# Kernel tuning notes

Measured on AMD Instinct MI355X. Metric: run time of the kernel, lower is better.

The kernel has to match this reference:

```python
import jax, jax.numpy as jnp
import numpy as np

N_PE = 100000   # num 'pe' nodes
N_R = 100000    # num 'router' nodes
E = 600000      # edges per relation
D_IN = 64       # input feature dim per node type
H = 128         # hidden_channels
G = 64          # graphs in batch


def setup_inputs() -> dict:
    key = jax.random.key(0)
    ks = jax.random.split(key, 20)
    inp = {}
    inp["x_pe"] = jax.random.normal(ks[0], (N_PE, D_IN), jnp.float32)
    inp["x_r"] = jax.random.normal(ks[1], (N_R, D_IN), jnp.float32)
    # edge_index per relation: row0 = src node ids, row1 = dst node ids
    inp["ei_per"] = jax.random.randint(ks[2], (2, E), 0, N_PE, jnp.int32)   # pe -> router
    inp["ei_rpe"] = jax.random.randint(ks[3], (2, E), 0, N_R, jnp.int32)    # router -> pe
    inp["ei_rr"] = jax.random.randint(ks[4], (2, E), 0, N_R, jnp.int32)     # router -> router
    inp["batch_pe"] = jnp.sort(jax.random.randint(ks[5], (N_PE,), 0, G, jnp.int32))
    inp["batch_r"] = jnp.sort(jax.random.randint(ks[6], (N_R,), 0, G, jnp.int32))
    # GraphConv params, relation axis ordered [pe->router, router->pe, router->router]
    s1 = 1.0 / np.sqrt(D_IN)
    s2 = 1.0 / np.sqrt(H)
    inp["Wrel1"] = jax.random.normal(ks[7], (3, D_IN, H), jnp.float32) * s1
    inp["brel1"] = jnp.zeros((3, H), jnp.float32)
    inp["Wroot1"] = jax.random.normal(ks[8], (3, D_IN, H), jnp.float32) * s1
    inp["Wrel23"] = jax.random.normal(ks[9], (2, 3, H, H), jnp.float32) * s2
    inp["brel23"] = jnp.zeros((2, 3, H), jnp.float32)
    inp["Wroot23"] = jax.random.normal(ks[10], (2, 3, H, H), jnp.float32) * s2
    # per-node-type MLP heads, type axis ordered [pe, router]
    inp["mlp_W1"] = jax.random.normal(ks[11], (2, H, 5), jnp.float32) * s2
    inp["mlp_b1"] = jnp.zeros((2, 5), jnp.float32)
    inp["mlp_W2"] = jax.random.normal(ks[12], (2, 5, 1), jnp.float32) * (1.0 / np.sqrt(5.0))
    inp["mlp_b2"] = jnp.zeros((2, 1), jnp.float32)
    inp["out_W"] = jax.random.normal(ks[13], (2, 1), jnp.float32) * (1.0 / np.sqrt(2.0))
    inp["out_b"] = jnp.zeros((1,), jnp.float32)
    return inp


def _hetero_graphconv(x_pe, x_r, ei_per, ei_rpe, ei_rr, Wrel, brel, Wroot):
    # GraphConv: lin_rel(scatter_add(x_src)) + lin_root(x_dst); to_hetero sums per dst type.
    agg_r_from_pe = jax.ops.segment_sum(x_pe[ei_per[0]], ei_per[1], num_segments=N_R)
    agg_pe_from_r = jax.ops.segment_sum(x_r[ei_rpe[0]], ei_rpe[1], num_segments=N_PE)
    agg_r_from_r = jax.ops.segment_sum(x_r[ei_rr[0]], ei_rr[1], num_segments=N_R)
    o_pe = agg_pe_from_r @ Wrel[1] + brel[1] + x_pe @ Wroot[1]
    o_r = (agg_r_from_pe @ Wrel[0] + brel[0] + x_r @ Wroot[0]) \
        + (agg_r_from_r @ Wrel[2] + brel[2] + x_r @ Wroot[2])
    return o_pe, o_r


def reference(x_pe, x_r, ei_per, ei_rpe, ei_rr, batch_pe, batch_r,
              Wrel1, brel1, Wroot1, Wrel23, brel23, Wroot23,
              mlp_W1, mlp_b1, mlp_W2, mlp_b2, out_W, out_b):
    h_pe, h_r = _hetero_graphconv(x_pe, x_r, ei_per, ei_rpe, ei_rr, Wrel1, brel1, Wroot1)
    h_pe, h_r = jax.nn.relu(h_pe), jax.nn.relu(h_r)
    h_pe, h_r = _hetero_graphconv(h_pe, h_r, ei_per, ei_rpe, ei_rr, Wrel23[0], brel23[0], Wroot23[0])
    h_pe, h_r = jax.nn.relu(h_pe), jax.nn.relu(h_r)
    h_pe, h_r = _hetero_graphconv(h_pe, h_r, ei_per, ei_rpe, ei_rr, Wrel23[1], brel23[1], Wroot23[1])
    gm_pe = jax.ops.segment_max(h_pe, batch_pe, num_segments=G)  # [G, H]
    gm_r = jax.ops.segment_max(h_r, batch_r, num_segments=G)
    def mlp(x, W1, b1, W2, b2):
        return jax.nn.relu(x @ W1 + b1) @ W2 + b2
    o_pe = mlp(gm_pe, mlp_W1[0], mlp_b1[0], mlp_W2[0], mlp_b2[0])  # [G, 1]
    o_r = mlp(gm_r, mlp_W1[1], mlp_b1[1], mlp_W2[1], mlp_b2[1])
    cat = jnp.concatenate([o_pe, o_r], axis=1)  # [G, 2]
    return cat @ out_W + out_b  # [G, 1]
```

## Files before the change

kernel.cpp:

```cpp
#include <hip/hip_runtime.h>
#include <cstddef>
#include <cstdint>

#define DIN 64
#define HID 128
#define NBKMAX 256
#define EPB 8192

typedef _Float16 half4v __attribute__((ext_vector_type(4)));
typedef _Float16 half8v __attribute__((ext_vector_type(8)));
typedef float f32x16 __attribute__((ext_vector_type(16)));

__device__ __forceinline__ unsigned encf(float f) {
    unsigned b = __float_as_uint(f);
    return (b & 0x80000000u) ? ~b : (b | 0x80000000u);
}
__device__ __forceinline__ float decf(unsigned u) {
    unsigned b = (u & 0x80000000u) ? (u & 0x7FFFFFFFu) : ~u;
    return __uint_as_float(b);
}

__global__ void matadd3_k(const float* a0, const float* b0f, float* o0, int n0,
                          const float* a1, const float* b1f, float* o1, int n1,
                          const float* a2, const float* b2f, float* o2, int n2) {
    int r = blockIdx.y;
    const float* a = r == 0 ? a0 : (r == 1 ? a1 : a2);
    const float* b = r == 0 ? b0f : (r == 1 ? b1f : b2f);
    float* o = r == 0 ? o0 : (r == 1 ? o1 : o2);
    int n = r == 0 ? n0 : (r == 1 ? n1 : n2);
    int i = blockIdx.x * 256 + threadIdx.x;
    if (i < n) o[i] = a[i] + b[i];
}

__global__ void conv_x2_k(const float* s0, _Float16* d0, int n40,
                          const float* s1, _Float16* d1, int n41) {
    int r = blockIdx.y;
    const float* s = r == 0 ? s0 : s1;
    _Float16* d = r == 0 ? d0 : d1;
    int n4 = r == 0 ? n40 : n41;
    int i = blockIdx.x * 256 + threadIdx.x;
    if (i >= n4) return;
    float4 v = *reinterpret_cast<const float4*>(&s[i * 4]);
    half4v h;
    h.x = (_Float16)v.x; h.y = (_Float16)v.y; h.z = (_Float16)v.z; h.w = (_Float16)v.w;
    *reinterpret_cast<half4v*>(&d[i * 4]) = h;
}

struct CW { const float* src; _Float16* dst; int K; int total; };
__global__ void conv_w7_k(CW c0, CW c1, CW c2, CW c3, CW c4, CW c5, CW c6) {
    CW J;
    switch (blockIdx.y) {
        case 0: J = c0; break; case 1: J = c1; break; case 2: J = c2; break;
        case 3: J = c3; break; case 4: J = c4; break; case 5: J = c5; break;
        default: J = c6; break;
    }
    int i = blockIdx.x * 256 + threadIdx.x;
    if (i >= J.total) return;
    int m = i / (J.K * HID);
    int rem = i % (J.K * HID);
    int k = rem / HID;
    int col = rem % HID;
    J.dst[(size_t)m * HID * J.K + (size_t)col * J.K + k] = (_Float16)J.src[i];
}

__global__ __launch_bounds__(256) void bhist_k(const int* e0, const int* e1, const int* e2, int E,
                                               int* c0, int* c1, int* c2) {
    int r = blockIdx.y;
    const int* ei = r == 0 ? e0 : (r == 1 ? e1 : e2);
    int* cnt = r == 0 ? c0 : (r == 1 ? c1 : c2);
    __shared__ int sc[NBKMAX];
    int t = threadIdx.x;
    sc[t] = 0;
    __syncthreads();
    int base = blockIdx.x * EPB;
    int n = min(EPB, E - base);
    for (int i = t; i < n; i += 256)
        atomicAdd(&sc[(unsigned)ei[E + base + i] >> 9], 1);
    __syncthreads();
    if (sc[t]) atomicAdd(&cnt[t], sc[t]);
}

__global__ __launch_bounds__(256) void bscan_k(int* c0, int* bb0, int* cu0, int* rp0, int n0,
                                               int* c1, int* bb1, int* cu1, int* rp1, int n1,
                                               int* c2, int* bb2, int* cu2, int* rp2, int n2,
                                               int E) {
    __shared__ int sh[256];
    int t = threadIdx.x;
    for (int r = 0; r < 3; ++r) {
        int* cnt = r == 0 ? c0 : (r == 1 ? c1 : c2);
        int* bb  = r == 0 ? bb0 : (r == 1 ? bb1 : bb2);
        int* cu  = r == 0 ? cu0 : (r == 1 ? cu1 : cu2);
        int* rp  = r == 0 ? rp0 : (r == 1 ? rp1 : rp2);
        int N    = r == 0 ? n0 : (r == 1 ? n1 : n2);
        int v = cnt[t];
        sh[t] = v;
        __syncthreads();
        for (int off = 1; off < 256; off <<= 1) {
            int val = (t >= off) ? sh[t - off] : 0;
            __syncthreads();
            sh[t] += val;
            __syncthreads();
        }
        int ex = sh[t] - v;
        bb[t] = ex;
        cu[t] = ex;
        if (t == 255) bb[256] = sh[255];
        if (t == 0) rp[N] = E;
        __syncthreads();
    }
}

__global__ __launch_bounds__(256) void bin_k(const int* e0, const int* e1, const int* e2, int E,
                                             int* cu0, int* cu1, int* cu2,
                                             unsigned* t0, unsigned* t1, unsigned* t2) {
    int r = blockIdx.y;
    const int* ei = r == 0 ? e0 : (r == 1 ? e1 : e2);
    int* gcur = r == 0 ? cu0 : (r == 1 ? cu1 : cu2);
    unsigned* temp = r == 0 ? t0 : (r == 1 ? t1 : t2);
    __shared__ unsigned pk[EPB];
    __shared__ unsigned short bkb[EPB];
    __shared__ int cnt[NBKMAX];
    __shared__ int scn[NBKMAX];
    __shared__ int rb[NBKMAX];
    int t = threadIdx.x;
    int base = blockIdx.x * EPB;
    int n = min(EPB, E - base);
    cnt[t] = 0;
    __syncthreads();
    for (int i = t; i < n; i += 256)
        atomicAdd(&cnt[(unsigned)ei[E + base + i] >> 9], 1);
    __syncthreads();
    {
        int v = cnt[t];
        scn[t] = v;
        __syncthreads();
        for (int off = 1; off < 256; off <<= 1) {
            int val = (t >= off) ? scn[t - off] : 0;
            __syncthreads();
            scn[t] += val;
            __syncthreads();
        }
        int ex = scn[t] - v;
        __syncthreads();
        scn[t] = ex;
    }
    {
        int c = cnt[t];
        rb[t] = c ? atomicAdd(&gcur[t], c) : 0;
        cnt[t] = 0;
    }
    __syncthreads();
    for (int i = t; i < n; i += 256) {
        int s = ei[base + i];
        int d = ei[E + base + i];
        int b = (unsigned)d >> 9;
        int slot = scn[b] + atomicAdd(&cnt[b], 1);
        pk[slot] = ((unsigned)s << 9) | (unsigned)(d & 511);
        bkb[slot] = (unsigned short)b;
    }
    __syncthreads();
    for (int i = t; i < n; i += 256) {
        int b = bkb[i];
        temp[rb[b] + (i - scn[b])] = pk[i];
    }
}

__global__ __launch_bounds__(256) void bcsr_k(const unsigned* t0, const unsigned* t1, const unsigned* t2,
                                              const int* bb0, const int* bb1, const int* bb2,
                                              int* rp0, int* rp1, int* rp2,
                                              int* a0, int* a1, int* a2,
                                              int n0, int n1, int n2) {
    int r = blockIdx.y;
    const unsigned* temp = r == 0 ? t0 : (r == 1 ? t1 : t2);
    const int* bb = r == 0 ? bb0 : (r == 1 ? bb1 : bb2);
    int* rp = r == 0 ? rp0 : (r == 1 ? rp1 : rp2);
    int* adj = r == 0 ? a0 : (r == 1 ? a1 : a2);
    int N = r == 0 ? n0 : (r == 1 ? n1 : n2);
    int b = blockIdx.x;
    int lo = bb[b], hi = bb[b + 1];
    __shared__ int cnt[512];
    __shared__ int sh[256];
    int t = threadIdx.x;
    cnt[t] = 0; cnt[t + 256] = 0;
    __syncthreads();
    for (int i = lo + t; i < hi; i += 256)
        atomicAdd(&cnt[temp[i] & 511], 1);
    __syncthreads();
    int c0 = cnt[2 * t], c1 = cnt[2 * t + 1];
    sh[t] = c0 + c1;
    __syncthreads();
    for (int off = 1; off < 256; off <<= 1) {
        int v = (t >= off) ? sh[t - off] : 0;
        __syncthreads();
        sh[t] += v;
        __syncthreads();
    }
    int pairExcl = sh[t] - (c0 + c1);
    __syncthreads();
    int e0x = lo + pairExcl;
    int e1x = e0x + c0;
    cnt[2 * t] = e0x;
    cnt[2 * t + 1] = e1x;
    int nodeBase = b * 512;
    if (nodeBase + 2 * t < N) rp[nodeBase + 2 * t] = e0x;
    if (nodeBase + 2 * t + 1 < N) rp[nodeBase + 2 * t + 1] = e1x;
    __syncthreads();
    for (int i = lo + t; i < hi; i += 256) {
        unsigned p = temp[i];
        int pos = atomicAdd(&cnt[p & 511], 1);
        adj[pos] = p >> 9;
    }
}

struct AJob { const _Float16* X; const int* rp; const int* adj; _Float16* AGG; int N; int gb; };
template <int D>
__global__ __launch_bounds__(256) void gather3_k(AJob a0, AJob a1, AJob a2) {
    int b = blockIdx.x;
    AJob J;
    if (b < a0.gb) { J = a0; }
    else if (b < a0.gb + a1.gb) { J = a1; b -= a0.gb; }
    else { J = a2; b -= a0.gb + a1.gb; }
    constexpr int TPN = D / 8;
    constexpr int NPB = 256 / TPN;
    int node = b * NPB + threadIdx.x / TPN;
    int lane = threadIdx.x % TPN;
    if (node >= J.N) return;
    int a = J.rp[node], e1 = J.rp[node + 1];
    float acc[8] = {0.f, 0.f, 0.f, 0.f, 0.f, 0.f, 0.f, 0.f};
    int e = a;
    for (; e + 2 <= e1; e += 2) {
        int s0 = J.adj[e], s1 = J.adj[e + 1];
        half8v v0 = *reinterpret_cast<const half8v*>(&J.X[(size_t)s0 * D + lane * 8]);
        half8v v1 = *reinterpret_cast<const half8v*>(&J.X[(size_t)s1 * D + lane * 8]);
#pragma unroll
        for (int i = 0; i < 8; ++i) acc[i] += (float)v0[i];
#pragma unroll
        for (int i = 0; i < 8; ++i) acc[i] += (float)v1[i];
    }
    if (e < e1) {
        int s0 = J.adj[e];
        half8v v0 = *reinterpret_cast<const half8v*>(&J.X[(size_t)s0 * D + lane * 8]);
#pragma unroll
        for (int i = 0; i < 8; ++i) acc[i] += (float)v0[i];
    }
    half8v o;
#pragma unroll
    for (int i = 0; i < 8; ++i) o[i] = (_Float16)acc[i];
    *reinterpret_cast<half8v*>(&J.AGG[(size_t)node * D + lane * 8]) = o;
}

struct GJob {
    const _Float16* A0; const _Float16* A1; const _Float16* A2;
    const _Float16* W0; const _Float16* W1; const _Float16* W2;
    const float* b0; const float* b1;
    _Float16* O;
    int N; int total; int gb;
};

template <bool RELU>
__global__ __launch_bounds__(256) void gemm2_k(GJob j0, GJob j1, int K, int lg) {
    const bool second = ((int)blockIdx.x >= j0.gb);
    const GJob J = second ? j1 : j0;
    const int bx = blockIdx.x - (second ? j0.gb : 0);
    __shared__ _Float16 Alds[2][128 * 32];
    const int tid = threadIdx.x;
    const int lane = tid & 63;
    const int w = tid >> 6;
    const int wr = w & 1, wc = w >> 1;
    const int rowBase = bx * 128;

    f32x16 acc[2][2];
#pragma unroll
    for (int r = 0; r < 2; ++r)
#pragma unroll
        for (int c = 0; c < 2; ++c)
#pragma unroll
            for (int q = 0; q < 16; ++q) acc[r][c][q] = 0.0f;

    const _Float16* Ap[3] = {J.A0, J.A1, J.A2};

    const int srow = tid & 127;
    const int skh = (tid >> 7) * 16;
    const int gr = rowBase + srow;
    const bool rowOK = (gr < J.N);
    const int sR = (srow >> 5) * 2 + (skh >> 4);
    const int sl5 = srow & 31;
    const int off0 = (sR * 64 + sl5) * 8;
    const int off1 = (sR * 64 + sl5 + 32) * 8;

    const int total = J.total;
    const int cmask = (1 << lg) - 1;

    auto ld = [&](int c, half8v& h0, half8v& h1) {
        int s = c >> lg;
        int k0 = (c & cmask) * 32;
        half8v z = {};
        h0 = z; h1 = z;
        if (rowOK) {
            const _Float16* p = Ap[s] + (size_t)gr * K + k0 + skh;
            h0 = *reinterpret_cast<const half8v*>(p);
            h1 = *reinterpret_cast<const half8v*>(p + 8);
        }
    };

    half8v pa, pb, na, nb, fa, fb;
    ld(0, pa, pb);
    *reinterpret_cast<half8v*>(&Alds[0][off0]) = pa;
    *reinterpret_cast<half8v*>(&Alds[0][off1]) = pb;
    if (total > 1) ld(1, na, nb);
    __syncthreads();

    for (int c = 0; c < total; ++c) {
        if (c + 2 < total) ld(c + 2, fa, fb);
        int s = c >> lg;
        int k0 = (c & cmask) * 32;
        const _Float16* __restrict__ Wt = (s == 0) ? J.W0 : (s == 1 ? J.W1 : J.W2);
        const _Float16* buf = Alds[c & 1];
#pragma unroll
        for (int t = 0; t < 2; ++t) {
            half8v av[2], wv[2];
#pragma unroll
            for (int r = 0; r < 2; ++r) {
                int R = (wr * 2 + r) * 2 + t;
                av[r] = *reinterpret_cast<const half8v*>(&buf[(R * 64 + lane) * 8]);
            }
#pragma unroll
            for (int cc = 0; cc < 2; ++cc) {
                int col = wc * 64 + cc * 32 + (lane & 31);
                wv[cc] = *reinterpret_cast<const half8v*>(
                    &Wt[(size_t)col * K + k0 + t * 16 + (lane >> 5) * 8]);
            }
#pragma unroll
            for (int r = 0; r < 2; ++r)
#pragma unroll
                for (int cc = 0; cc < 2; ++cc)
                    acc[r][cc] = __builtin_amdgcn_mfma_f32_32x32x16_f16(wv[cc], av[r], acc[r][cc], 0, 0, 0);
        }
        if (c + 1 < total) {
            _Float16* nbuf = Alds[(c + 1) & 1];
            *reinterpret_cast<half8v*>(&nbuf[off0]) = na;
            *reinterpret_cast<half8v*>(&nbuf[off1]) = nb;
        }
        __syncthreads();
        na = fa; nb = fb;
    }

#pragma unroll
    for (int r = 0; r < 2; ++r) {
        int node = rowBase + (wr * 2 + r) * 32 + (lane & 31);
        if (node >= J.N) continue;
        _Float16* orow = J.O + (size_t)node * HID;
#pragma unroll
        for (int cc = 0; cc < 2; ++cc) {
            int fb_ = wc * 64 + cc * 32 + 4 * (lane >> 5);
#pragma unroll
            for (int g = 0; g < 4; ++g) {
                int f = fb_ + g * 8;
                float4 bv = *reinterpret_cast<const float4*>(&J.b0[f]);
                if (J.b1) {
                    float4 b2v = *reinterpret_cast<const float4*>(&J.b1[f]);
                    bv.x += b2v.x; bv.y += b2v.y; bv.z += b2v.z; bv.w += b2v.w;
                }
                half4v hv;
#pragma unroll
                for (int i = 0; i < 4; ++i) {
                    float v = acc[r][cc][g * 4 + i] + ((const float*)&bv)[i];
                    if (RELU) v = fmaxf(v, 0.f);
                    hv[i] = (_Float16)v;
                }
                *reinterpret_cast<half4v*>(&orow[f]) = hv;
            }
        }
    }
}

__global__ void seg_bounds2_k(const int* b0, int n0, int* s0,
                              const int* b1, int n1, int* s1, int G) {
    int r = blockIdx.x;
    const int* batch = r == 0 ? b0 : b1;
    int n = r == 0 ? n0 : n1;
    int* starts = r == 0 ? s0 : s1;
    int g = threadIdx.x;
    if (g > G) return;
    int lo = 0, hi = n;
    while (lo < hi) {
        int mid = (lo + hi) >> 1;
        if (batch[mid] < g) lo = mid + 1; else hi = mid;
    }
    starts[g] = lo;
}

__global__ __launch_bounds__(128) void seg_max2_k(const _Float16* H0, const int* st0, unsigned* g0,
                                                  const _Float16* H1, const int* st1, unsigned* g1) {
    int z = blockIdx.z;
    const _Float16* Hf = z == 0 ? H0 : H1;
    const int* starts = z == 0 ? st0 : st1;
    unsigned* gmU = z == 0 ? g0 : g1;
    int g = blockIdx.x;
    int sub = blockIdx.y;
    int SUB = gridDim.y;
    int f = threadIdx.x;
    int s0 = starts[g], s1 = starts[g + 1];
    int len = s1 - s0;
    if (len <= 0) return;
    int chunk = (len + SUB - 1) / SUB;
    int a = s0 + sub * chunk;
    int b = min(a + chunk, s1);
    if (a >= b) return;
    float m = -__builtin_huge_valf();
    for (int n = a; n < b; ++n) m = fmaxf(m, (float)Hf[(size_t)n * HID + f]);
    atomicMax(&gmU[g * HID + f], encf(m));
}

__global__ void head_k(const unsigned* __restrict__ gmU_pe, const unsigned* __restrict__ gmU_r,
                       const float* __restrict__ W1, const float* __restrict__ b1,
                       const float* __restrict__ W2, const float* __restrict__ b2,
                       const float* __restrict__ oW, const float* __restrict__ ob,
                       float* __restrict__ out, int G) {
    int g = threadIdx.x;
    if (g >= G) return;
    float vals[2];
#pragma unroll
    for (int t = 0; t < 2; ++t) {
        const unsigned* gm = t ? gmU_r : gmU_pe;
        float z[5];
#pragma unroll
        for (int j = 0; j < 5; ++j) z[j] = b1[t * 5 + j];
        for (int f = 0; f < HID; ++f) {
            float x = decf(gm[g * HID + f]);
#pragma unroll
            for (int j = 0; j < 5; ++j) z[j] = fmaf(x, W1[t * HID * 5 + f * 5 + j], z[j]);
        }
        float o = b2[t];
#pragma unroll
        for (int j = 0; j < 5; ++j) o = fmaf(fmaxf(z[j], 0.f), W2[t * 5 + j], o);
        vals[t] = o;
    }
    out[g] = vals[0] * oW[0] + vals[1] * oW[1] + ob[0];
}

extern "C" void kernel_launch(void* const* d_in, const int* in_sizes, int n_in,
                              void* d_out, int out_size, void* d_ws, size_t ws_size,
                              hipStream_t stream) {
    const float* x_pe    = (const float*)d_in[0];
    const float* x_r     = (const float*)d_in[1];
    const int* ei_per    = (const int*)d_in[2];
    const int* ei_rpe    = (const int*)d_in[3];
    const int* ei_rr     = (const int*)d_in[4];
    const int* batch_pe  = (const int*)d_in[5];
    const int* batch_r   = (const int*)d_in[6];
    const float* Wrel1   = (const float*)d_in[7];
    const float* brel1   = (const float*)d_in[8];
    const float* Wroot1  = (const float*)d_in[9];
    const float* Wrel23  = (const float*)d_in[10];
    const float* brel23  = (const float*)d_in[11];
    const float* Wroot23 = (const float*)d_in[12];
    const float* mlp_W1  = (const float*)d_in[13];
    const float* mlp_b1  = (const float*)d_in[14];
    const float* mlp_W2  = (const float*)d_in[15];
    const float* mlp_b2  = (const float*)d_in[16];
    const float* out_W   = (const float*)d_in[17];
    const float* out_b   = (const float*)d_in[18];
    float* out = (float*)d_out;

    const int N_PE = in_sizes[0] / DIN;
    const int N_R  = in_sizes[1] / DIN;
    const int E    = in_sizes[2] / 2;
    const int G    = out_size;
    const int NMAX = (N_PE > N_R) ? N_PE : N_R;
    const size_t SZM = (size_t)NMAX * HID;

    _Float16* H1 = (_Float16*)d_ws;
    _Float16* H2 = H1 + SZM;
    _Float16* H3 = H2 + SZM;
    _Float16* H4 = H3 + SZM;
    _Float16* H5 = H4 + SZM;
    _Float16* xh_pe = H5 + SZM;
    _Float16* xh_r  = xh_pe + (size_t)N_PE * DIN;
    float* wsum1 = (float*)(xh_r + (size_t)N_R * DIN);
    float* wsum2 = wsum1 + DIN * HID;
    float* wsum3 = wsum2 + HID * HID;
    _Float16* wt_rel1    = (_Float16*)(wsum3 + HID * HID);
    _Float16* wt_root1pe = wt_rel1 + 3 * DIN * HID;
    _Float16* wt_wsum1   = wt_root1pe + DIN * HID;
    _Float16* wt_rel23   = wt_wsum1 + DIN * HID;
    _Float16* wt_root23  = wt_rel23 + 6 * HID * HID;
    _Float16* wt_wsum2   = wt_root23 + 6 * HID * HID;
    _Float16* wt_wsum3   = wt_wsum2 + HID * HID;
    unsigned* gmU_pe = (unsigned*)(wt_wsum3 + HID * HID);
    unsigned* gmU_r  = gmU_pe + G * HID;
    int* starts_pe = (int*)(gmU_r + G * HID);
    int* starts_r  = starts_pe + (G + 1);
    int* bktCnt = starts_r + (G + 1);
    int* bb     = bktCnt + 3 * NBKMAX;
    int* gcur   = bb + 3 * (NBKMAX + 1);
    int* csr    = gcur + 3 * NBKMAX;
    const size_t relstride = (size_t)(NMAX + 1) + 2 * (size_t)E + 16;

    int* rp[3]; int* adjp[3]; unsigned* tmp[3];
    const int Nds[3] = {N_R, N_PE, N_R};
    for (int r = 0; r < 3; ++r) {
        int* rowptr = csr + (size_t)r * relstride;
        rp[r] = rowptr;
        adjp[r] = rowptr + (Nds[r] + 1);
        tmp[r] = (unsigned*)(adjp[r] + E);
    }

    const int gpe = (N_PE + 127) / 128, grr = (N_R + 127) / 128;

    {
        dim3 g((16384 + 255) / 256, 3);
        matadd3_k<<<g, 256, 0, stream>>>(
            Wroot1, Wroot1 + 2 * DIN * HID, wsum1, DIN * HID,
            Wroot23, Wroot23 + 2 * HID * HID, wsum2, HID * HID,
            Wroot23 + 3 * HID * HID, Wroot23 + 5 * HID * HID, wsum3, HID * HID);
    }
    {
        int n40 = N_PE * DIN / 4, n41 = N_R * DIN / 4;
        int nmax = n40 > n41 ? n40 : n41;
        dim3 g((nmax + 255) / 256, 2);
        conv_x2_k<<<g, 256, 0, stream>>>(x_pe, xh_pe, n40, x_r, xh_r, n41);
    }
    {
        CW c0{Wrel1, wt_rel1, DIN, 3 * DIN * HID};
        CW c1{Wroot1 + 1 * DIN * HID, wt_root1pe, DIN, DIN * HID};
        CW c2{wsum1, wt_wsum1, DIN, DIN * HID};
        CW c3{Wrel23, wt_rel23, HID, 6 * HID * HID};
        CW c4{Wroot23, wt_root23, HID, 6 * HID * HID};
        CW c5{wsum2, wt_wsum2, HID, HID * HID};
        CW c6{wsum3, wt_wsum3, HID, HID * HID};
        dim3 g((6 * HID * HID + 255) / 256, 7);
        conv_w7_k<<<g, 256, 0, stream>>>(c0, c1, c2, c3, c4, c5, c6);
    }
    {
        hipMemsetAsync(bktCnt, 0, 3 * NBKMAX * sizeof(int), stream);
        int eb = (E + EPB - 1) / EPB;
        dim3 gh(eb, 3);
        bhist_k<<<gh, 256, 0, stream>>>(ei_per, ei_rpe, ei_rr, E,
                                        bktCnt, bktCnt + NBKMAX, bktCnt + 2 * NBKMAX);
        bscan_k<<<1, 256, 0, stream>>>(
            bktCnt, bb, gcur, rp[0], Nds[0],
            bktCnt + NBKMAX, bb + (NBKMAX + 1), gcur + NBKMAX, rp[1], Nds[1],
            bktCnt + 2 * NBKMAX, bb + 2 * (NBKMAX + 1), gcur + 2 * NBKMAX, rp[2], Nds[2], E);
        bin_k<<<gh, 256, 0, stream>>>(ei_per, ei_rpe, ei_rr, E,
                                      gcur, gcur + NBKMAX, gcur + 2 * NBKMAX,
                                      tmp[0], tmp[1], tmp[2]);
        dim3 gc(NBKMAX, 3);
        bcsr_k<<<gc, 256, 0, stream>>>(tmp[0], tmp[1], tmp[2],
                                       bb, bb + (NBKMAX + 1), bb + 2 * (NBKMAX + 1),
                                       rp[0], rp[1], rp[2],
                                       adjp[0], adjp[1], adjp[2],
                                       Nds[0], Nds[1], Nds[2]);
    }

    {
        AJob a0{xh_r, rp[1], adjp[1], H1, N_PE, (N_PE + 31) / 32};
        AJob a1{xh_pe, rp[0], adjp[0], H2, N_R, (N_R + 31) / 32};
        AJob a2{xh_r, rp[2], adjp[2], H3, N_R, (N_R + 31) / 32};
        gather3_k<DIN><<<a0.gb + a1.gb + a2.gb, 256, 0, stream>>>(a0, a1, a2);
        GJob jp{H1, xh_pe, nullptr,
                wt_rel1 + 1 * DIN * HID, wt_root1pe, nullptr,
                brel1 + HID, nullptr, H4, N_PE, 2 * 2, gpe};
        GJob jr{H2, H3, xh_r,
                wt_rel1, wt_rel1 + 2 * DIN * HID, wt_wsum1,
                brel1, brel1 + 2 * HID, H5, N_R, 3 * 2, grr};
        gemm2_k<true><<<gpe + grr, 256, 0, stream>>>(jp, jr, DIN, 1);
    }
    {
        AJob a0{H5, rp[1], adjp[1], H1, N_PE, (N_PE + 15) / 16};
        AJob a1{H4, rp[0], adjp[0], H2, N_R, (N_R + 15) / 16};
        AJob a2{H5, rp[2], adjp[2], H3, N_R, (N_R + 15) / 16};
        gather3_k<HID><<<a0.gb + a1.gb + a2.gb, 256, 0, stream>>>(a0, a1, a2);
        GJob jp{H1, H4, nullptr,
                wt_rel23 + 1 * HID * HID, wt_root23 + 1 * HID * HID, nullptr,
                brel23 + HID, nullptr, H1, N_PE, 2 * 4, gpe};
        GJob jr{H2, H3, H5,
                wt_rel23, wt_rel23 + 2 * HID * HID, wt_wsum2,
                brel23, brel23 + 2 * HID, H2, N_R, 3 * 4, grr};
        gemm2_k<true><<<gpe + grr, 256, 0, stream>>>(jp, jr, HID, 2);
    }
    {
        AJob a0{H2, rp[1], adjp[1], H3, N_PE, (N_PE + 15) / 16};
        AJob a1{H1, rp[0], adjp[0], H4, N_R, (N_R + 15) / 16};
        AJob a2{H2, rp[2], adjp[2], H5, N_R, (N_R + 15) / 16};
        gather3_k<HID><<<a0.gb + a1.gb + a2.gb, 256, 0, stream>>>(a0, a1, a2);
        GJob jp{H3, H1, nullptr,
                wt_rel23 + 4 * HID * HID, wt_root23 + 4 * HID * HID, nullptr,
                brel23 + 4 * HID, nullptr, H3, N_PE, 2 * 4, gpe};
        GJob jr{H4, H5, H2,
                wt_rel23 + 3 * HID * HID, wt_rel23 + 5 * HID * HID, wt_wsum3,
                brel23 + 3 * HID, brel23 + 5 * HID, H4, N_R, 3 * 4, grr};
        gemm2_k<false><<<gpe + grr, 256, 0, stream>>>(jp, jr, HID, 2);
    }

    seg_bounds2_k<<<2, 128, 0, stream>>>(batch_pe, N_PE, starts_pe, batch_r, N_R, starts_r, G);
    hipMemsetAsync(gmU_pe, 0, 2 * (size_t)G * HID * sizeof(unsigned), stream);
    dim3 gs(G, 16, 2);
    seg_max2_k<<<gs, 128, 0, stream>>>(H3, starts_pe, gmU_pe, H4, starts_r, gmU_r);
    head_k<<<1, 64, 0, stream>>>(gmU_pe, gmU_r, mlp_W1, mlp_b1, mlp_W2, mlp_b2, out_W, out_b, out, G);
}
```

Baseline: 643.2 us.

## Fuse CSR neighbor gather into GEMM kernel, staging aggregates in LDS

Replaces the separate gather kernel plus GEMM with one fused kernel per layer. Each block gathers neighbor sums for its 128 destination rows directly into shared memory and then runs the MFMA GEMM against each relation's weight, with no aggregate round-trip through global memory. This removes the writes and re-reads of the aggregated feature buffers and one launch per layer. In exchange it drops the double-buffered A prefetch, so the irregular gather and the MFMA work now run in serialized phases. LDS use per block also grows to the full 128xK tile (32 KB for K=128), which may lower occupancy.

```diff
diff --git a/kernel.cpp b/kernel.cpp
--- a/kernel.cpp
+++ b/kernel.cpp
@@ -212,57 +212,25 @@
     }
 }
 
-struct AJob { const _Float16* X; const int* rp; const int* adj; _Float16* AGG; int N; int gb; };
-template <int D>
-__global__ __launch_bounds__(256) void gather3_k(AJob a0, AJob a1, AJob a2) {
-    int b = blockIdx.x;
-    AJob J;
-    if (b < a0.gb) { J = a0; }
-    else if (b < a0.gb + a1.gb) { J = a1; b -= a0.gb; }
-    else { J = a2; b -= a0.gb + a1.gb; }
-    constexpr int TPN = D / 8;
-    constexpr int NPB = 256 / TPN;
-    int node = b * NPB + threadIdx.x / TPN;
-    int lane = threadIdx.x % TPN;
-    if (node >= J.N) return;
-    int a = J.rp[node], e1 = J.rp[node + 1];
-    float acc[8] = {0.f, 0.f, 0.f, 0.f, 0.f, 0.f, 0.f, 0.f};
-    int e = a;
-    for (; e + 2 <= e1; e += 2) {
-        int s0 = J.adj[e], s1 = J.adj[e + 1];
-        half8v v0 = *reinterpret_cast<const half8v*>(&J.X[(size_t)s0 * D + lane * 8]);
-        half8v v1 = *reinterpret_cast<const half8v*>(&J.X[(size_t)s1 * D + lane * 8]);
-#pragma unroll
-        for (int i = 0; i < 8; ++i) acc[i] += (float)v0[i];
-#pragma unroll
-        for (int i = 0; i < 8; ++i) acc[i] += (float)v1[i];
-    }
-    if (e < e1) {
-        int s0 = J.adj[e];
-        half8v v0 = *reinterpret_cast<const half8v*>(&J.X[(size_t)s0 * D + lane * 8]);
-#pragma unroll
-        for (int i = 0; i < 8; ++i) acc[i] += (float)v0[i];
-    }
-    half8v o;
-#pragma unroll
-    for (int i = 0; i < 8; ++i) o[i] = (_Float16)acc[i];
-    *reinterpret_cast<half8v*>(&J.AGG[(size_t)node * D + lane * 8]) = o;
-}
-
-struct GJob {
-    const _Float16* A0; const _Float16* A1; const _Float16* A2;
-    const _Float16* W0; const _Float16* W1; const _Float16* W2;
+struct FJob {
+    const _Float16* X0; const int* rp0; const int* adj0; const _Float16* W0;
+    const _Float16* X1; const int* rp1; const int* adj1; const _Float16* W1;
+    const _Float16* X2; const int* rp2; const int* adj2; const _Float16* W2;
     const float* b0; const float* b1;
     _Float16* O;
-    int N; int total; int gb;
+    int N; int nsrc; int gb;
 };
 
-template <bool RELU>
-__global__ __launch_bounds__(256) void gemm2_k(GJob j0, GJob j1, int K, int lg) {
+template <int K, bool RELU>
+__global__ __launch_bounds__(256) void fgemm_k(FJob j0, FJob j1) {
+    constexpr int KS = K / 16;
+    constexpr int TPN = K / 8;
+    constexpr int NPB = 256 / TPN;
+    __shared__ _Float16 Alds[128 * K];
+
     const bool second = ((int)blockIdx.x >= j0.gb);
-    const GJob J = second ? j1 : j0;
+    const FJob J = second ? j1 : j0;
     const int bx = blockIdx.x - (second ? j0.gb : 0);
-    __shared__ _Float16 Alds[2][128 * 32];
     const int tid = threadIdx.x;
     const int lane = tid & 63;
     const int w = tid >> 6;
@@ -277,58 +245,67 @@
 #pragma unroll
             for (int q = 0; q < 16; ++q) acc[r][c][q] = 0.0f;
 
-    const _Float16* Ap[3] = {J.A0, J.A1, J.A2};
-
-    const int srow = tid & 127;
-    const int skh = (tid >> 7) * 16;
-    const int gr = rowBase + srow;
-    const bool rowOK = (gr < J.N);
-    const int sR = (srow >> 5) * 2 + (skh >> 4);
-    const int sl5 = srow & 31;
-    const int off0 = (sR * 64 + sl5) * 8;
-    const int off1 = (sR * 64 + sl5 + 32) * 8;
-
-    const int total = J.total;
-    const int cmask = (1 << lg) - 1;
-
-    auto ld = [&](int c, half8v& h0, half8v& h1) {
-        int s = c >> lg;
-        int k0 = (c & cmask) * 32;
-        half8v z = {};
-        h0 = z; h1 = z;
-        if (rowOK) {
-            const _Float16* p = Ap[s] + (size_t)gr * K + k0 + skh;
-            h0 = *reinterpret_cast<const half8v*>(p);
-            h1 = *reinterpret_cast<const half8v*>(p + 8);
+    const int nloc = tid / TPN;
+    const int glane = tid % TPN;
+    const int gt = glane >> 1;
+    const int gk8 = glane & 1;
+
+    for (int s = 0; s < J.nsrc; ++s) {
+        const _Float16* X; const int* rp; const int* adj; const _Float16* Wt;
+        if (s == 0) { X = J.X0; rp = J.rp0; adj = J.adj0; Wt = J.W0; }
+        else if (s == 1) { X = J.X1; rp = J.rp1; adj = J.adj1; Wt = J.W1; }
+        else { X = J.X2; rp = J.rp2; adj = J.adj2; Wt = J.W2; }
+
+#pragma unroll
+        for (int pass = 0; pass < 128 / NPB; ++pass) {
+            int row = pass * NPB + nloc;
+            int node = rowBase + row;
+            half8v h = {};
+            if (node < J.N) {
+                if (rp) {
+                    int a = rp[node], b = rp[node + 1];
+                    float av[8] = {0.f, 0.f, 0.f, 0.f, 0.f, 0.f, 0.f, 0.f};
+                    int e = a;
+                    for (; e + 2 <= b; e += 2) {
+                        int s0 = adj[e], s1 = adj[e + 1];
+                        half8v v0 = *reinterpret_cast<const half8v*>(&X[(size_t)s0 * K + glane * 8]);
+                        half8v v1 = *reinterpret_cast<const half8v*>(&X[(size_t)s1 * K + glane * 8]);
+#pragma unroll
+                        for (int i = 0; i < 8; ++i) av[i] += (float)v0[i];
+#pragma unroll
+                        for (int i = 0; i < 8; ++i) av[i] += (float)v1[i];
+                    }
+                    if (e < b) {
+                        int s0 = adj[e];
+                        half8v v0 = *reinterpret_cast<const half8v*>(&X[(size_t)s0 * K + glane * 8]);
+#pragma unroll
+                        for (int i = 0; i < 8; ++i) av[i] += (float)v0[i];
+                    }
+#pragma unroll
+                    for (int i = 0; i < 8; ++i) h[i] = (_Float16)av[i];
+                } else {
+                    h = *reinterpret_cast<const half8v*>(&X[(size_t)node * K + glane * 8]);
+                }
+            }
+            int R = (row >> 5) * KS + gt;
+            int l = (row & 31) + 32 * gk8;
+            *reinterpret_cast<half8v*>(&Alds[(R * 64 + l) * 8]) = h;
         }
-    };
-
-    half8v pa, pb, na, nb, fa, fb;
-    ld(0, pa, pb);
-    *reinterpret_cast<half8v*>(&Alds[0][off0]) = pa;
-    *reinterpret_cast<half8v*>(&Alds[0][off1]) = pb;
-    if (total > 1) ld(1, na, nb);
-    __syncthreads();
-
-    for (int c = 0; c < total; ++c) {
-        if (c + 2 < total) ld(c + 2, fa, fb);
-        int s = c >> lg;
-        int k0 = (c & cmask) * 32;
-        const _Float16* __restrict__ Wt = (s == 0) ? J.W0 : (s == 1 ? J.W1 : J.W2);
-        const _Float16* buf = Alds[c & 1];
-#pragma unroll
-        for (int t = 0; t < 2; ++t) {
+        __syncthreads();
+
+#pragma unroll
+        for (int t = 0; t < KS; ++t) {
             half8v av[2], wv[2];
 #pragma unroll
             for (int r = 0; r < 2; ++r) {
-                int R = (wr * 2 + r) * 2 + t;
-                av[r] = *reinterpret_cast<const half8v*>(&buf[(R * 64 + lane) * 8]);
+                int R = (wr * 2 + r) * KS + t;
+                av[r] = *reinterpret_cast<const half8v*>(&Alds[(R * 64 + lane) * 8]);
             }
 #pragma unroll
             for (int cc = 0; cc < 2; ++cc) {
                 int col = wc * 64 + cc * 32 + (lane & 31);
                 wv[cc] = *reinterpret_cast<const half8v*>(
-                    &Wt[(size_t)col * K + k0 + t * 16 + (lane >> 5) * 8]);
+                    &Wt[(size_t)col * K + t * 16 + (lane >> 5) * 8]);
             }
 #pragma unroll
             for (int r = 0; r < 2; ++r)
@@ -336,13 +313,7 @@
                 for (int cc = 0; cc < 2; ++cc)
                     acc[r][cc] = __builtin_amdgcn_mfma_f32_32x32x16_f16(wv[cc], av[r], acc[r][cc], 0, 0, 0);
         }
-        if (c + 1 < total) {
-            _Float16* nbuf = Alds[(c + 1) & 1];
-            *reinterpret_cast<half8v*>(&nbuf[off0]) = na;
-            *reinterpret_cast<half8v*>(&nbuf[off1]) = nb;
-        }
-        __syncthreads();
-        na = fa; nb = fb;
+        __syncthreads();
     }
 
 #pragma unroll
@@ -554,43 +525,37 @@
     }
 
     {
-        AJob a0{xh_r, rp[1], adjp[1], H1, N_PE, (N_PE + 31) / 32};
-        AJob a1{xh_pe, rp[0], adjp[0], H2, N_R, (N_R + 31) / 32};
-        AJob a2{xh_r, rp[2], adjp[2], H3, N_R, (N_R + 31) / 32};
-        gather3_k<DIN><<<a0.gb + a1.gb + a2.gb, 256, 0, stream>>>(a0, a1, a2);
-        GJob jp{H1, xh_pe, nullptr,
-                wt_rel1 + 1 * DIN * HID, wt_root1pe, nullptr,
-                brel1 + HID, nullptr, H4, N_PE, 2 * 2, gpe};
-        GJob jr{H2, H3, xh_r,
-                wt_rel1, wt_rel1 + 2 * DIN * HID, wt_wsum1,
-                brel1, brel1 + 2 * HID, H5, N_R, 3 * 2, grr};
-        gemm2_k<true><<<gpe + grr, 256, 0, stream>>>(jp, jr, DIN, 1);
-    }
-    {
-        AJob a0{H5, rp[1], adjp[1], H1, N_PE, (N_PE + 15) / 16};
-        AJob a1{H4, rp[0], adjp[0], H2, N_R, (N_R + 15) / 16};
-        AJob a2{H5, rp[2], adjp[2], H3, N_R, (N_R + 15) / 16};
-        gather3_k<HID><<<a0.gb + a1.gb + a2.gb, 256, 0, stream>>>(a0, a1, a2);
-        GJob jp{H1, H4, nullptr,
-                wt_rel23 + 1 * HID * HID, wt_root23 + 1 * HID * HID, nullptr,
-                brel23 + HID, nullptr, H1, N_PE, 2 * 4, gpe};
-        GJob jr{H2, H3, H5,
-                wt_rel23, wt_rel23 + 2 * HID * HID, wt_wsum2,
-                brel23, brel23 + 2 * HID, H2, N_R, 3 * 4, grr};
-        gemm2_k<true><<<gpe + grr, 256, 0, stream>>>(jp, jr, HID, 2);
-    }
-    {
-        AJob a0{H2, rp[1], adjp[1], H3, N_PE, (N_PE + 15) / 16};
-        AJob a1{H1, rp[0], adjp[0], H4, N_R, (N_R + 15) / 16};
-        AJob a2{H2, rp[2], adjp[2], H5, N_R, (N_R + 15) / 16};
-        gather3_k<HID><<<a0.gb + a1.gb + a2.gb, 256, 0, stream>>>(a0, a1, a2);
-        GJob jp{H3, H1, nullptr,
-                wt_rel23 + 4 * HID * HID, wt_root23 + 4 * HID * HID, nullptr,
-                brel23 + 4 * HID, nullptr, H3, N_PE, 2 * 4, gpe};
-        GJob jr{H4, H5, H2,
-                wt_rel23 + 3 * HID * HID, wt_rel23 + 5 * HID * HID, wt_wsum3,
-                brel23 + 3 * HID, brel23 + 5 * HID, H4, N_R, 3 * 4, grr};
-        gemm2_k<false><<<gpe + grr, 256, 0, stream>>>(jp, jr, HID, 2);
+        FJob jp{xh_r, rp[1], adjp[1], wt_rel1 + 1 * DIN * HID,
+                xh_pe, nullptr, nullptr, wt_root1pe,
+                nullptr, nullptr, nullptr, nullptr,
+                brel1 + HID, nullptr, H4, N_PE, 2, gpe};
+        FJob jr{xh_pe, rp[0], adjp[0], wt_rel1,
+                xh_r, rp[2], adjp[2], wt_rel1 + 2 * DIN * HID,
+                xh_r, nullptr, nullptr, wt_wsum1,
+                brel1, brel1 + 2 * HID, H5, N_R, 3, grr};
+        fgemm_k<DIN, true><<<gpe + grr, 256, 0, stream>>>(jp, jr);
+    }
+    {
+        FJob jp{H5, rp[1], adjp[1], wt_rel23 + 1 * HID * HID,
+                H4, nullptr, nullptr, wt_root23 + 1 * HID * HID,
+                nullptr, nullptr, nullptr, nullptr,
+                brel23 + HID, nullptr, H1, N_PE, 2, gpe};
+        FJob jr{H4, rp[0], adjp[0], wt_rel23,
+                H5, rp[2], adjp[2], wt_rel23 + 2 * HID * HID,
+                H5, nullptr, nullptr, wt_wsum2,
+                brel23, brel23 + 2 * HID, H2, N_R, 3, grr};
+        fgemm_k<HID, true><<<gpe + grr, 256, 0, stream>>>(jp, jr);
+    }
+    {
+        FJob jp{H2, rp[1], adjp[1], wt_rel23 + 4 * HID * HID,
+                H1, nullptr, nullptr, wt_root23 + 4 * HID * HID,
+                nullptr, nullptr, nullptr, nullptr,
+                brel23 + 4 * HID, nullptr, H3, N_PE, 2, gpe};
+        FJob jr{H1, rp[0], adjp[0], wt_rel23 + 3 * HID * HID,
+                H2, rp[2], adjp[2], wt_rel23 + 5 * HID * HID,
+                H2, nullptr, nullptr, wt_wsum3,
+                brel23 + 3 * HID, brel23 + 5 * HID, H4, N_R, 3, grr};
+        fgemm_k<HID, false><<<gpe + grr, 256, 0, stream>>>(jp, jr);
     }
 
     seg_bounds2_k<<<2, 128, 0, stream>>>(batch_pe, N_PE, starts_pe, batch_r, N_R, starts_r, G);
```

New measurement: 787.4 us. 1.22x slower.
